# Performance work log

Measured on AMD Instinct MI355X. Metric: run time of the kernel, lower is better.

Reference implementation:

```python
import jax, jax.numpy as jnp
import numpy as np

SCALE = 1.0 / np.sqrt(3.0)  # head dim is input_dim = 3


def setup_inputs() -> dict:
    key = jax.random.key(0)
    ks = jax.random.split(key, 7)
    B, Nq, Nf, D, C = 4, 2048, 16384, 3, 768
    return {
        "q": jax.random.normal(ks[0], (B, Nq, D), dtype=jnp.float32),
        "k": jax.random.normal(ks[1], (B, Nf, D), dtype=jnp.float32),
        "v": jax.random.normal(ks[2], (B, Nf, C), dtype=jnp.float32),
        "W1": jax.random.normal(ks[3], (D, D), dtype=jnp.float32) * (1.0 / np.sqrt(D)),
        "b1": jax.random.normal(ks[4], (D,), dtype=jnp.float32) * 0.01,
        "W2": jax.random.normal(ks[5], (D, D), dtype=jnp.float32) * (1.0 / np.sqrt(D)),
        "b2": jax.random.normal(ks[6], (D,), dtype=jnp.float32) * 0.01,
    }


def reference(q, k, v, W1, b1, W2, b2):
    # tiny per-point projections + ReLU (nn.Linear stores W as [out,in] -> x @ W.T + b)
    qp = jax.nn.relu(jnp.einsum("bnd,ed->bne", q, W1) + b1)  # [B, Nq, 3]
    kp = jax.nn.relu(jnp.einsum("bmd,ed->bme", k, W2) + b2)  # [B, Nf, 3]
    scores = jnp.einsum("bne,bme->bnm", qp, kp) * SCALE       # [B, Nq, Nf]
    attn = jax.nn.softmax(scores, axis=-1)
    return jnp.einsum("bnm,bmc->bnc", attn, v)                # [B, Nq, C]
```

## Files before the change

### kernel.cpp

```cpp
#include <hip/hip_runtime.h>
#include <math.h>

#define Bt  4
#define NQ  2048
#define NF  16384
#define CC  768

#define QT  128
#define CT  96
#define BK  128
#define THR 512
#define NCH (NF / BK)

#define NFS   4
#define KC    (NF / NFS)
#define BK2   16
#define NCH2  (KC / BK2)
#define TILEB (CC * BK2 * 2)
#define NTILE (Bt * (NF / BK2))

#define SCALE_LOG2E 0.8329080161227079f

typedef __attribute__((ext_vector_type(8)))  short  short8;
typedef __attribute__((ext_vector_type(4)))  float  floatx4;
typedef __attribute__((ext_vector_type(16))) float  floatx16;

#if __has_builtin(__builtin_amdgcn_exp2f)
#define EXP2F(x) __builtin_amdgcn_exp2f(x)
#else
#define EXP2F(x) __expf((x) * 0.6931471805599453f)
#endif

static __device__ __forceinline__ float relu(float x) { return fmaxf(x, 0.0f); }

static __device__ __forceinline__ unsigned int f2bf(float f) {
    unsigned int u = __float_as_uint(f);
    u += 0x7fffu + ((u >> 16) & 1u);
    return u >> 16;
}

#define GLDS16(gsrc, ldst)                                                        \
    __builtin_amdgcn_global_load_lds(                                             \
        (const __attribute__((address_space(1))) unsigned int*)(gsrc),            \
        (__attribute__((address_space(3))) unsigned int*)(ldst), 16, 0, 0)

__global__ __launch_bounds__(256) void prep_kernel(
    const float* __restrict__ q, const float* __restrict__ k,
    const float* __restrict__ W1, const float* __restrict__ b1,
    const float* __restrict__ W2, const float* __restrict__ b2,
    float4* __restrict__ qp, float* __restrict__ kp3)
{
    int idx = blockIdx.x * 256 + threadIdx.x;
    if (idx < Bt * NQ) {
        const float* r = q + (size_t)idx * 3;
        float x0 = r[0], x1 = r[1], x2 = r[2];
        float4 o;
        o.x = relu(fmaf(W1[0], x0, fmaf(W1[1], x1, fmaf(W1[2], x2, b1[0])))) * SCALE_LOG2E;
        o.y = relu(fmaf(W1[3], x0, fmaf(W1[4], x1, fmaf(W1[5], x2, b1[1])))) * SCALE_LOG2E;
        o.z = relu(fmaf(W1[6], x0, fmaf(W1[7], x1, fmaf(W1[8], x2, b1[2])))) * SCALE_LOG2E;
        o.w = 0.0f;
        qp[idx] = o;
    } else {
        int kidx = idx - Bt * NQ;
        const float* r = k + (size_t)kidx * 3;
        float x0 = r[0], x1 = r[1], x2 = r[2];
        float* dst = kp3 + (size_t)kidx * 3;
        dst[0] = relu(fmaf(W2[0], x0, fmaf(W2[1], x1, fmaf(W2[2], x2, b2[0]))));
        dst[1] = relu(fmaf(W2[3], x0, fmaf(W2[4], x1, fmaf(W2[5], x2, b2[1]))));
        dst[2] = relu(fmaf(W2[6], x0, fmaf(W2[7], x1, fmaf(W2[8], x2, b2[2]))));
    }
}

__global__ __launch_bounds__(256) void stats_kernel(
    float4* __restrict__ qp, const float* __restrict__ kp3,
    float2* __restrict__ rstat)
{
    __shared__ float wredA[4][16];
    __shared__ float wredB[4][16];

    const int bid  = blockIdx.x;
    const int b    = bid >> 7;
    const int q0   = (bid & 127) * 16;
    const int t    = threadIdx.x;
    const int wv   = t >> 6;
    const int lane = t & 63;

    float qx[16], qy[16], qz[16];
#pragma unroll
    for (int i = 0; i < 16; ++i) {
        float4 qv = qp[b * NQ + q0 + i];
        qx[i] = qv.x; qy[i] = qv.y; qz[i] = qv.z;
    }
    const float* kpb = kp3 + (size_t)b * NF * 3;

    float pmax[16];
#pragma unroll
    for (int i = 0; i < 16; ++i) pmax[i] = -1e30f;
    for (int m = t; m < NF; m += 256) {
        float kx = kpb[3 * m], ky = kpb[3 * m + 1], kz = kpb[3 * m + 2];
#pragma unroll
        for (int i = 0; i < 16; ++i) {
            float s = fmaf(qx[i], kx, fmaf(qy[i], ky, qz[i] * kz));
            pmax[i] = fmaxf(pmax[i], s);
        }
    }
#pragma unroll
    for (int off = 32; off >= 1; off >>= 1)
#pragma unroll
        for (int i = 0; i < 16; ++i)
            pmax[i] = fmaxf(pmax[i], __shfl_xor(pmax[i], off, 64));
    if (lane == 0)
#pragma unroll
        for (int i = 0; i < 16; ++i) wredA[wv][i] = pmax[i];
    __syncthreads();

    float rowmax[16];
#pragma unroll
    for (int i = 0; i < 16; ++i)
        rowmax[i] = fmaxf(fmaxf(wredA[0][i], wredA[1][i]),
                          fmaxf(wredA[2][i], wredA[3][i]));

    float psum[16];
#pragma unroll
    for (int i = 0; i < 16; ++i) psum[i] = 0.0f;
    for (int m = t; m < NF; m += 256) {
        float kx = kpb[3 * m], ky = kpb[3 * m + 1], kz = kpb[3 * m + 2];
#pragma unroll
        for (int i = 0; i < 16; ++i) {
            float s = fmaf(qx[i], kx, fmaf(qy[i], ky, qz[i] * kz));
            psum[i] += EXP2F(s - rowmax[i]);
        }
    }
#pragma unroll
    for (int off = 32; off >= 1; off >>= 1)
#pragma unroll
        for (int i = 0; i < 16; ++i)
            psum[i] += __shfl_xor(psum[i], off, 64);
    if (lane == 0)
#pragma unroll
        for (int i = 0; i < 16; ++i) wredB[wv][i] = psum[i];
    __syncthreads();

    if (t < 16) {
        float m = fmaxf(fmaxf(wredA[0][t], wredA[1][t]),
                        fmaxf(wredA[2][t], wredA[3][t]));
        float l = wredB[0][t] + wredB[1][t] + wredB[2][t] + wredB[3][t];
        int row = b * NQ + q0 + t;
        rstat[row] = make_float2(m, 1.0f / l);
        qp[row].w = -m;
    }
}

__global__ __launch_bounds__(256) void prep_v_kernel(
    const float* __restrict__ v, char* __restrict__ vpk)
{
    __shared__ float lt[16][132];
    const int t   = threadIdx.x;
    const int bid = blockIdx.x;
    const int cb  = bid % 6;
    const int ch  = (bid / 6) & 1023;
    const int b   = bid / (6 * 1024);
    const int c0  = cb * 128;

    const float* vb = v + ((size_t)b * NF + (size_t)ch * BK2) * CC + c0;
    const int c4 = (t & 31) * 4;
#pragma unroll
    for (int r2 = 0; r2 < 2; ++r2) {
        const int row = (t >> 5) + 8 * r2;
        *(float4*)&lt[row][c4] = *(const float4*)(vb + (size_t)row * CC + c4);
    }
    __syncthreads();

    const int c  = t >> 1;
    const int sl = t & 1;
    unsigned int dw[4];
#pragma unroll
    for (int i = 0; i < 4; ++i) {
        float a  = lt[8 * sl + 2 * i][c];
        float b2 = lt[8 * sl + 2 * i + 1][c];
        asm("v_cvt_pk_bf16_f32 %0, %1, %2" : "=v"(dw[i]) : "v"(a), "v"(b2));
    }
    const int cgl = c0 + c;
    char* dst = vpk + (size_t)(b * (NF / BK2) + ch) * TILEB
              + ((size_t)cgl << 5)
              + ((sl ^ ((cgl >> 2) & 1)) << 4);
    uint4 u; u.x = dw[0]; u.y = dw[1]; u.z = dw[2]; u.w = dw[3];
    *(uint4*)dst = u;
}

static __device__ __forceinline__ void produceA(
    const float* __restrict__ kpq,
    float qx, float qy, float qz, float qw,
    int l, int cg, unsigned int (*ab)[64][2])
{
    float2 a0 = *(const float2*)(kpq);
    float2 a1 = *(const float2*)(kpq + 2);
    float2 a2 = *(const float2*)(kpq + 4);
    float2 b0 = *(const float2*)(kpq + 24);
    float2 b1 = *(const float2*)(kpq + 26);
    float2 b2 = *(const float2*)(kpq + 28);
    float e0 = EXP2F(fmaf(qx, a0.x, fmaf(qy, a0.y, fmaf(qz, a1.x, qw))));
    float e1 = EXP2F(fmaf(qx, a1.y, fmaf(qy, a2.x, fmaf(qz, a2.y, qw))));
    float e2 = EXP2F(fmaf(qx, b0.x, fmaf(qy, b0.y, fmaf(qz, b1.x, qw))));
    float e3 = EXP2F(fmaf(qx, b1.y, fmaf(qy, b2.x, fmaf(qz, b2.y, qw))));
    unsigned int d0, d1;
    asm("v_cvt_pk_bf16_f32 %0, %1, %2" : "=v"(d0) : "v"(e0), "v"(e1));
    asm("v_cvt_pk_bf16_f32 %0, %1, %2" : "=v"(d1) : "v"(e2), "v"(e3));
    asm("v_permlane32_swap_b32 %0, %1" : "+v"(d0), "+v"(d1));
    ab[cg >> 1][l][cg & 1]       = d0;
    ab[(cg >> 1) + 2][l][cg & 1] = d1;
}

__global__ __launch_bounds__(256, 2) void attn_main32_kernel(
    const char* __restrict__ vpk, const float4* __restrict__ qp,
    const float* __restrict__ kp3, float* __restrict__ out,
    float* __restrict__ partial)
{
    __shared__ __align__(16) char vbuf[2][TILEB];
    __shared__ __align__(16) unsigned int abuf[2][4][64][2];

    const int t   = threadIdx.x;
    const int l   = t & 63;
    const int cg  = t >> 6;

    const int bid = blockIdx.x;
    const int g   = ((bid & 7) << 1) | ((bid >> 3) & 1);
    const int qt  = bid >> 4;
    const int b   = g >> 2;
    const int nfs = g & 3;

    const char*  vtile = vpk + (size_t)(b * (NF / BK2) + nfs * NCH2) * TILEB;
    const float* kpb   = kp3 + (size_t)(b * NF + nfs * KC) * 3;

    const float4 qv = qp[b * NQ + qt * 64 + l];
    const float qx = qv.x, qy = qv.y, qz = qv.z, qw = qv.w;

    floatx16 acc0[6], acc1[6];
#pragma unroll
    for (int cs = 0; cs < 6; ++cs)
#pragma unroll
        for (int r = 0; r < 16; ++r) { acc0[cs][r] = 0.0f; acc1[cs][r] = 0.0f; }

    const int lhi  = l >> 5;
    const int bofs = (cg * 192 + (l & 31)) * 32 + ((lhi ^ ((l >> 2) & 1)) << 4);

#define STAGE(CH, PB)                                                         \
    do {                                                                      \
        const char* src = vtile + (size_t)(CH) * TILEB + cg * 6144 + l * 16;  \
        char* dst = &vbuf[PB][cg * 6144];                                     \
        _Pragma("unroll")                                                     \
        for (int i = 0; i < 6; ++i) GLDS16(src + i * 1024, dst + i * 1024);   \
    } while (0)

    STAGE(0, 0);
    produceA(kpb + 6 * cg, qx, qy, qz, qw, l, cg, abuf[0]);

#pragma unroll 1
    for (int ch = 0; ch < NCH2; ++ch) {
        asm volatile("s_waitcnt vmcnt(0) lgkmcnt(0)" ::: "memory");
        __builtin_amdgcn_sched_barrier(0);
        __builtin_amdgcn_s_barrier();
        __builtin_amdgcn_sched_barrier(0);

        const int cur = ch & 1, nxt = cur ^ 1;
        if (ch + 1 < NCH2) STAGE(ch + 1, nxt);

        union { unsigned int u[4]; short8 s; } a0, a1;
        {
            const unsigned int (*AB)[64][2] = abuf[cur];
            uint2 p0 = *(const uint2*)&AB[0][l][0];
            uint2 p1 = *(const uint2*)&AB[1][l][0];
            uint2 p2 = *(const uint2*)&AB[2][l][0];
            uint2 p3 = *(const uint2*)&AB[3][l][0];
            a0.u[0] = p0.x; a0.u[1] = p0.y; a0.u[2] = p1.x; a0.u[3] = p1.y;
            a1.u[0] = p2.x; a1.u[1] = p2.y; a1.u[2] = p3.x; a1.u[3] = p3.y;
        }

        const char* bp = &vbuf[cur][0] + bofs;
        __builtin_amdgcn_s_setprio(1);
#pragma unroll
        for (int cs = 0; cs < 6; ++cs) {
            union { uint4 u; short8 s; } bw;
            bw.u = *(const uint4*)(bp + cs * 1024);
            acc0[cs] = __builtin_amdgcn_mfma_f32_32x32x16_bf16(a0.s, bw.s, acc0[cs], 0, 0, 0);
            acc1[cs] = __builtin_amdgcn_mfma_f32_32x32x16_bf16(a1.s, bw.s, acc1[cs], 0, 0, 0);
        }
        __builtin_amdgcn_s_setprio(0);

        if (ch + 1 < NCH2)
            produceA(kpb + (size_t)(ch + 1) * (BK2 * 3) + 6 * cg,
                     qx, qy, qz, qw, l, cg, abuf[nxt]);
    }
#undef STAGE

    float* obase = (nfs == 0) ? out
                 : (partial + (size_t)(nfs - 1) * ((size_t)Bt * NQ * CC));
    const int row0 = b * NQ + qt * 64 + 4 * lhi;
    const int col0 = cg * 192 + (l & 31);
#pragma unroll
    for (int cs = 0; cs < 6; ++cs)
#pragma unroll
        for (int r = 0; r < 16; ++r) {
            const int row = row0 + (r & 3) + 8 * (r >> 2);
            obase[(size_t)row * CC + col0 + cs * 32]        = acc0[cs][r];
            obase[(size_t)(row + 32) * CC + col0 + cs * 32] = acc1[cs][r];
        }
}

__global__ __launch_bounds__(256) void reduce_kernel(
    float* __restrict__ out, const float* __restrict__ part,
    const float2* __restrict__ rstat)
{
    const int TOT4 = Bt * NQ * CC / 4;
    float4* o4 = (float4*)out;
    const float4* p4 = (const float4*)part;
    for (int i = blockIdx.x * 256 + threadIdx.x; i < TOT4; i += gridDim.x * 256) {
        float4 o = o4[i];
        float4 a = p4[i], b2 = p4[TOT4 + i], c2 = p4[2 * TOT4 + i];
        float lv = rstat[i / (CC / 4)].y;
        o.x = (o.x + a.x + b2.x + c2.x) * lv;
        o.y = (o.y + a.y + b2.y + c2.y) * lv;
        o.z = (o.z + a.z + b2.z + c2.z) * lv;
        o.w = (o.w + a.w + b2.w + c2.w) * lv;
        o4[i] = o;
    }
}

__global__ __launch_bounds__(THR, 4) void attn_mfma_kernel(
    const float* __restrict__ v, const float4* __restrict__ qp,
    const float* __restrict__ kp3, const float2* __restrict__ rstat,
    float* __restrict__ out)
{
    __shared__ unsigned int vTd[2][CT * 68];
    __shared__ float4 kplB[2][96];

    const int t    = threadIdx.x;
    const int bid  = blockIdx.x;
    const int g    = (bid & 7) + 8 * ((bid >> 3) & 3);
    const int qt   = bid >> 5;
    const int b    = g >> 3;
    const int ct   = g & 7;

    const int lane = t & 63;
    const int wv   = t >> 6;
    const int quad = lane >> 4;
    const int l15  = lane & 15;

    const int qrow0 = b * NQ + qt * QT;
    const int cbase = ct * CT;

    float4 qv = qp[qrow0 + wv * 16 + l15];
    const float qx = qv.x, qy = qv.y, qz = qv.z, qw = qv.w;

    const int rp  = (t & 7) + 8 * wv;
    const int c4l = (t >> 3) & 7;

    const float*  vb   = v + (size_t)b * NF * CC + cbase;
    const float4* kp4g = (const float4*)(kp3 + (size_t)b * NF * 3);

    floatx4 acc[6];
#pragma unroll
    for (int cs = 0; cs < 6; ++cs) acc[cs] = (floatx4){0.f, 0.f, 0.f, 0.f};

    float va0[3][4], va1[3][4];
    float4 kpld = make_float4(0.f, 0.f, 0.f, 0.f);

#pragma unroll
    for (int rep = 0; rep < 3; ++rep) {
        int col = 4 * (c4l + 8 * rep);
        const float4* p0 = (const float4*)(vb + (size_t)(2 * rp) * CC + col);
        float4 a = p0[0];
        float4 bq = p0[CC / 4];
        va0[rep][0] = a.x;  va0[rep][1] = a.y;  va0[rep][2] = a.z;  va0[rep][3] = a.w;
        va1[rep][0] = bq.x; va1[rep][1] = bq.y; va1[rep][2] = bq.z; va1[rep][3] = bq.w;
    }
    if (t < 96) kpld = kp4g[t];

    for (int ch = 0; ch < NCH; ++ch) {
        const int p = ch & 1;
#pragma unroll
        for (int rep = 0; rep < 3; ++rep) {
            int c0 = 4 * (c4l + 8 * rep);
#pragma unroll
            for (int w = 0; w < 4; ++w) {
                unsigned int pk = f2bf(va0[rep][w]) | (f2bf(va1[rep][w]) << 16);
                vTd[p][(c0 + w) * 68 + (rp ^ (4 * c4l))] = pk;
            }
        }
        if (t < 96) kplB[p][t] = kpld;
        __syncthreads();

        if (ch + 1 < NCH) {
            int m0 = (ch + 1) * BK;
#pragma unroll
            for (int rep = 0; rep < 3; ++rep) {
                int col = 4 * (c4l + 8 * rep);
                const float4* p0 = (const float4*)(vb + (size_t)(m0 + 2 * rp) * CC + col);
                float4 a = p0[0];
                float4 bq = p0[CC / 4];
                va0[rep][0] = a.x;  va0[rep][1] = a.y;  va0[rep][2] = a.z;  va0[rep][3] = a.w;
                va1[rep][0] = bq.x; va1[rep][1] = bq.y; va1[rep][2] = bq.z; va1[rep][3] = bq.w;
            }
            if (t < 96) kpld = kp4g[(ch + 1) * 96 + t];
        }

#pragma unroll
        for (int kk = 0; kk < BK; kk += 32) {
            union { float4 v4[6]; float f[24]; } kq;
            const int kb4 = (kk * 3) / 4 + 6 * quad;
#pragma unroll
            for (int i = 0; i < 6; ++i) kq.v4[i] = kplB[p][kb4 + i];

            union { short8 s; unsigned int d[4]; } af;
#pragma unroll
            for (int j = 0; j < 8; j += 2) {
                float s0 = fmaf(qx, kq.f[3 * j],
                           fmaf(qy, kq.f[3 * j + 1],
                           fmaf(qz, kq.f[3 * j + 2], qw)));
                float s1 = fmaf(qx, kq.f[3 * j + 3],
                           fmaf(qy, kq.f[3 * j + 4],
                           fmaf(qz, kq.f[3 * j + 5], qw)));
                af.d[j >> 1] = f2bf(EXP2F(s0)) | (f2bf(EXP2F(s1)) << 16);
            }

#pragma unroll
            for (int cs = 0; cs < 6; ++cs) {
                int c  = cs * 16 + l15;
                int d0 = ((kk >> 1) + 4 * quad) ^ (4 * ((c >> 2) & 7));
                union { uint4 u; short8 s; } bw;
                bw.u = *(const uint4*)&vTd[p][c * 68 + d0];
                acc[cs] = __builtin_amdgcn_mfma_f32_16x16x32_bf16(
                    af.s, bw.s, acc[cs], 0, 0, 0);
            }
        }
        __syncthreads();
    }

#pragma unroll
    for (int vv = 0; vv < 4; ++vv) {
        int row = qrow0 + wv * 16 + quad * 4 + vv;
        float lv = rstat[row].y;
        float* orow = out + (size_t)row * CC + cbase + l15;
#pragma unroll
        for (int cs = 0; cs < 6; ++cs)
            orow[cs * 16] = acc[cs][vv] * lv;
    }
}

extern "C" void kernel_launch(void* const* d_in, const int* in_sizes, int n_in,
                              void* d_out, int out_size, void* d_ws, size_t ws_size,
                              hipStream_t stream) {
    const float* q  = (const float*)d_in[0];
    const float* k  = (const float*)d_in[1];
    const float* v  = (const float*)d_in[2];
    const float* W1 = (const float*)d_in[3];
    const float* b1 = (const float*)d_in[4];
    const float* W2 = (const float*)d_in[5];
    const float* b2 = (const float*)d_in[6];
    float* out = (float*)d_out;

    float*  kp3   = (float*)d_ws;
    float4* qpW   = (float4*)((char*)d_ws + (size_t)Bt * NF * 3 * 4);
    float2* rstat = (float2*)((char*)d_ws + (size_t)Bt * NF * 3 * 4 + (size_t)Bt * NQ * 16);
    char*   vpk   = (char*)d_ws + 983040;
    float*  part  = (float*)((char*)d_ws + 983040 + (size_t)NTILE * TILEB);
    const size_t need = 983040 + (size_t)NTILE * TILEB
                      + (size_t)3 * Bt * NQ * CC * 4;

    hipLaunchKernelGGL(prep_kernel, dim3((Bt * NQ + Bt * NF) / 256), dim3(256), 0, stream,
                       q, k, W1, b1, W2, b2, qpW, kp3);
    hipLaunchKernelGGL(stats_kernel, dim3(Bt * (NQ / 16)), dim3(256), 0, stream,
                       qpW, kp3, rstat);

    if (ws_size >= need) {
        hipLaunchKernelGGL(prep_v_kernel, dim3(Bt * (NF / BK2) * 6), dim3(256), 0, stream,
                           v, vpk);
        hipLaunchKernelGGL(attn_main32_kernel, dim3(Bt * 32 * NFS), dim3(256), 0, stream,
                           vpk, qpW, kp3, out, part);
        hipLaunchKernelGGL(reduce_kernel, dim3(2048), dim3(256), 0, stream,
                           out, part, rstat);
    } else {
        hipLaunchKernelGGL(attn_mfma_kernel, dim3(Bt * (NQ / QT) * (CC / CT)), dim3(THR), 0, stream,
                           v, qpW, kp3, rstat, out);
    }
}
```

Baseline: 743.3 us.

## Fuse softmax row sums into main kernel, widen blocks and triple-buffer V

Removes the separate stats kernel pass by accumulating the exp row sums inside the main MFMA kernel. These are written per split and combined and inverted in the reduce kernel. Blocks grow to 512 threads covering 128 query rows, so each staged V tile feeds twice as many rows. V staging is triple-buffered two chunks ahead, and the K loads for the next chunk are issued early into registers with partial vmcnt waits. The costs are more LDS, lower occupancy and fragile hand-counted waitcnt sequencing.

```diff
diff --git a/kernel.cpp b/kernel.cpp
--- a/kernel.cpp
+++ b/kernel.cpp
@@ -188,40 +188,20 @@
     *(uint4*)dst = u;
 }
 
-static __device__ __forceinline__ void produceA(
-    const float* __restrict__ kpq,
-    float qx, float qy, float qz, float qw,
-    int l, int cg, unsigned int (*ab)[64][2])
-{
-    float2 a0 = *(const float2*)(kpq);
-    float2 a1 = *(const float2*)(kpq + 2);
-    float2 a2 = *(const float2*)(kpq + 4);
-    float2 b0 = *(const float2*)(kpq + 24);
-    float2 b1 = *(const float2*)(kpq + 26);
-    float2 b2 = *(const float2*)(kpq + 28);
-    float e0 = EXP2F(fmaf(qx, a0.x, fmaf(qy, a0.y, fmaf(qz, a1.x, qw))));
-    float e1 = EXP2F(fmaf(qx, a1.y, fmaf(qy, a2.x, fmaf(qz, a2.y, qw))));
-    float e2 = EXP2F(fmaf(qx, b0.x, fmaf(qy, b0.y, fmaf(qz, b1.x, qw))));
-    float e3 = EXP2F(fmaf(qx, b1.y, fmaf(qy, b2.x, fmaf(qz, b2.y, qw))));
-    unsigned int d0, d1;
-    asm("v_cvt_pk_bf16_f32 %0, %1, %2" : "=v"(d0) : "v"(e0), "v"(e1));
-    asm("v_cvt_pk_bf16_f32 %0, %1, %2" : "=v"(d1) : "v"(e2), "v"(e3));
-    asm("v_permlane32_swap_b32 %0, %1" : "+v"(d0), "+v"(d1));
-    ab[cg >> 1][l][cg & 1]       = d0;
-    ab[(cg >> 1) + 2][l][cg & 1] = d1;
-}
-
-__global__ __launch_bounds__(256, 2) void attn_main32_kernel(
+__global__ __launch_bounds__(512) void attn_main32_kernel(
     const char* __restrict__ vpk, const float4* __restrict__ qp,
     const float* __restrict__ kp3, float* __restrict__ out,
-    float* __restrict__ partial)
+    float* __restrict__ partial, float* __restrict__ lpart)
 {
-    __shared__ __align__(16) char vbuf[2][TILEB];
-    __shared__ __align__(16) unsigned int abuf[2][4][64][2];
-
-    const int t   = threadIdx.x;
-    const int l   = t & 63;
-    const int cg  = t >> 6;
+    __shared__ __align__(16) char vbuf[3][TILEB];
+    __shared__ __align__(16) unsigned int abuf[2][2][4][64][2];
+    __shared__ float lred[2][4][64];
+
+    const int t  = threadIdx.x;
+    const int l  = t & 63;
+    const int wv = t >> 6;
+    const int wg = wv >> 2;
+    const int cg = wv & 3;
 
     const int bid = blockIdx.x;
     const int g   = ((bid & 7) << 1) | ((bid >> 3) & 1);
@@ -232,7 +212,7 @@
     const char*  vtile = vpk + (size_t)(b * (NF / BK2) + nfs * NCH2) * TILEB;
     const float* kpb   = kp3 + (size_t)(b * NF + nfs * KC) * 3;
 
-    const float4 qv = qp[b * NQ + qt * 64 + l];
+    const float4 qv = qp[b * NQ + qt * QT + wg * 64 + l];
     const float qx = qv.x, qy = qv.y, qz = qv.z, qw = qv.w;
 
     floatx16 acc0[6], acc1[6];
@@ -240,43 +220,87 @@
     for (int cs = 0; cs < 6; ++cs)
 #pragma unroll
         for (int r = 0; r < 16; ++r) { acc0[cs][r] = 0.0f; acc1[cs][r] = 0.0f; }
+
+    float lsum = 0.0f;
 
     const int lhi  = l >> 5;
     const int bofs = (cg * 192 + (l & 31)) * 32 + ((lhi ^ ((l >> 2) & 1)) << 4);
 
 #define STAGE(CH, PB)                                                         \
     do {                                                                      \
-        const char* src = vtile + (size_t)(CH) * TILEB + cg * 6144 + l * 16;  \
-        char* dst = &vbuf[PB][cg * 6144];                                     \
+        const char* src_ = vtile + (size_t)(CH) * TILEB + wv * 3072 + l * 16; \
+        char* dst_ = &vbuf[PB][wv * 3072];                                    \
         _Pragma("unroll")                                                     \
-        for (int i = 0; i < 6; ++i) GLDS16(src + i * 1024, dst + i * 1024);   \
+        for (int i_ = 0; i_ < 3; ++i_) GLDS16(src_ + i_ * 1024, dst_ + i_ * 1024); \
     } while (0)
 
-    STAGE(0, 0);
-    produceA(kpb + 6 * cg, qx, qy, qz, qw, l, cg, abuf[0]);
-
+#define KPLOAD(CH, R)                                                         \
+    do {                                                                      \
+        const float* p_ = kpb + (size_t)(CH) * (BK2 * 3) + 6 * cg;            \
+        asm volatile("global_load_dwordx2 %0, %6, off\n\t"                    \
+                     "global_load_dwordx2 %1, %6, off offset:8\n\t"           \
+                     "global_load_dwordx2 %2, %6, off offset:16\n\t"          \
+                     "global_load_dwordx2 %3, %6, off offset:96\n\t"          \
+                     "global_load_dwordx2 %4, %6, off offset:104\n\t"         \
+                     "global_load_dwordx2 %5, %6, off offset:112"             \
+                     : "=&v"(R[0]), "=&v"(R[1]), "=&v"(R[2]),                 \
+                       "=&v"(R[3]), "=&v"(R[4]), "=&v"(R[5])                  \
+                     : "v"(p_));                                              \
+    } while (0)
+
+#define PRODA(R, BB)                                                          \
+    do {                                                                      \
+        float e0_ = EXP2F(fmaf(qx, R[0].x, fmaf(qy, R[0].y, fmaf(qz, R[1].x, qw)))); \
+        float e1_ = EXP2F(fmaf(qx, R[1].y, fmaf(qy, R[2].x, fmaf(qz, R[2].y, qw)))); \
+        float e2_ = EXP2F(fmaf(qx, R[3].x, fmaf(qy, R[3].y, fmaf(qz, R[4].x, qw)))); \
+        float e3_ = EXP2F(fmaf(qx, R[4].y, fmaf(qy, R[5].x, fmaf(qz, R[5].y, qw)))); \
+        lsum += (e0_ + e1_) + (e2_ + e3_);                                    \
+        unsigned int d0_, d1_;                                                \
+        asm("v_cvt_pk_bf16_f32 %0, %1, %2" : "=v"(d0_) : "v"(e0_), "v"(e1_)); \
+        asm("v_cvt_pk_bf16_f32 %0, %1, %2" : "=v"(d1_) : "v"(e2_), "v"(e3_)); \
+        asm("v_permlane32_swap_b32 %0, %1" : "+v"(d0_), "+v"(d1_));           \
+        abuf[BB][wg][cg >> 1][l][cg & 1]       = d0_;                         \
+        abuf[BB][wg][(cg >> 1) + 2][l][cg & 1] = d1_;                         \
+    } while (0)
+
+    {
+        float2 kpr[6];
+        STAGE(0, 0);
+        STAGE(1, 1);
+        KPLOAD(0, kpr);
+        asm volatile("s_waitcnt vmcnt(0)" ::: "memory");
+        __builtin_amdgcn_sched_barrier(0);
+        PRODA(kpr, 0);
+    }
+
+    int p = 0;
 #pragma unroll 1
     for (int ch = 0; ch < NCH2; ++ch) {
-        asm volatile("s_waitcnt vmcnt(0) lgkmcnt(0)" ::: "memory");
+        asm volatile("s_waitcnt lgkmcnt(0)" ::: "memory");
         __builtin_amdgcn_sched_barrier(0);
         __builtin_amdgcn_s_barrier();
         __builtin_amdgcn_sched_barrier(0);
 
         const int cur = ch & 1, nxt = cur ^ 1;
-        if (ch + 1 < NCH2) STAGE(ch + 1, nxt);
+        float2 kpn[6];
+        if (ch + 1 < NCH2) KPLOAD(ch + 1, kpn);
+        if (ch + 2 < NCH2) {
+            const int p2 = (p + 2 >= 3) ? p + 2 - 3 : p + 2;
+            STAGE(ch + 2, p2);
+        }
+        __builtin_amdgcn_sched_barrier(0);
 
         union { unsigned int u[4]; short8 s; } a0, a1;
         {
-            const unsigned int (*AB)[64][2] = abuf[cur];
-            uint2 p0 = *(const uint2*)&AB[0][l][0];
-            uint2 p1 = *(const uint2*)&AB[1][l][0];
-            uint2 p2 = *(const uint2*)&AB[2][l][0];
-            uint2 p3 = *(const uint2*)&AB[3][l][0];
+            uint2 p0 = *(const uint2*)&abuf[cur][wg][0][l][0];
+            uint2 p1 = *(const uint2*)&abuf[cur][wg][1][l][0];
+            uint2 p2v = *(const uint2*)&abuf[cur][wg][2][l][0];
+            uint2 p3 = *(const uint2*)&abuf[cur][wg][3][l][0];
             a0.u[0] = p0.x; a0.u[1] = p0.y; a0.u[2] = p1.x; a0.u[3] = p1.y;
-            a1.u[0] = p2.x; a1.u[1] = p2.y; a1.u[2] = p3.x; a1.u[3] = p3.y;
-        }
-
-        const char* bp = &vbuf[cur][0] + bofs;
+            a1.u[0] = p2v.x; a1.u[1] = p2v.y; a1.u[2] = p3.x; a1.u[3] = p3.y;
+        }
+        const char* bp = &vbuf[p][0] + bofs;
+
         __builtin_amdgcn_s_setprio(1);
 #pragma unroll
         for (int cs = 0; cs < 6; ++cs) {
@@ -286,16 +310,30 @@
             acc1[cs] = __builtin_amdgcn_mfma_f32_32x32x16_bf16(a1.s, bw.s, acc1[cs], 0, 0, 0);
         }
         __builtin_amdgcn_s_setprio(0);
-
-        if (ch + 1 < NCH2)
-            produceA(kpb + (size_t)(ch + 1) * (BK2 * 3) + 6 * cg,
-                     qx, qy, qz, qw, l, cg, abuf[nxt]);
+        __builtin_amdgcn_sched_barrier(0);
+
+        if (ch + 1 < NCH2) {
+            if (ch + 2 < NCH2) asm volatile("s_waitcnt vmcnt(3)" ::: "memory");
+            else               asm volatile("s_waitcnt vmcnt(0)" ::: "memory");
+            __builtin_amdgcn_sched_barrier(0);
+            PRODA(kpn, nxt);
+        }
+        p = (p + 1 == 3) ? 0 : p + 1;
     }
 #undef STAGE
+#undef KPLOAD
+#undef PRODA
+
+    lred[wg][cg][l] = lsum;
+    __syncthreads();
+    if (cg == 0) {
+        float tot = lred[wg][0][l] + lred[wg][1][l] + lred[wg][2][l] + lred[wg][3][l];
+        lpart[(size_t)nfs * (Bt * NQ) + b * NQ + qt * QT + wg * 64 + l] = tot;
+    }
 
     float* obase = (nfs == 0) ? out
                  : (partial + (size_t)(nfs - 1) * ((size_t)Bt * NQ * CC));
-    const int row0 = b * NQ + qt * 64 + 4 * lhi;
+    const int row0 = b * NQ + qt * QT + wg * 64 + 4 * lhi;
     const int col0 = cg * 192 + (l & 31);
 #pragma unroll
     for (int cs = 0; cs < 6; ++cs)
@@ -309,15 +347,18 @@
 
 __global__ __launch_bounds__(256) void reduce_kernel(
     float* __restrict__ out, const float* __restrict__ part,
-    const float2* __restrict__ rstat)
+    const float* __restrict__ lpart)
 {
     const int TOT4 = Bt * NQ * CC / 4;
+    const int NROW = Bt * NQ;
     float4* o4 = (float4*)out;
     const float4* p4 = (const float4*)part;
     for (int i = blockIdx.x * 256 + threadIdx.x; i < TOT4; i += gridDim.x * 256) {
         float4 o = o4[i];
         float4 a = p4[i], b2 = p4[TOT4 + i], c2 = p4[2 * TOT4 + i];
-        float lv = rstat[i / (CC / 4)].y;
+        int row = i / (CC / 4);
+        float lv = 1.0f / (lpart[row] + lpart[NROW + row]
+                         + lpart[2 * NROW + row] + lpart[3 * NROW + row]);
         o.x = (o.x + a.x + b2.x + c2.x) * lv;
         o.y = (o.y + a.y + b2.y + c2.y) * lv;
         o.z = (o.z + a.z + b2.z + c2.z) * lv;
@@ -461,25 +502,26 @@
 
     float*  kp3   = (float*)d_ws;
     float4* qpW   = (float4*)((char*)d_ws + (size_t)Bt * NF * 3 * 4);
-    float2* rstat = (float2*)((char*)d_ws + (size_t)Bt * NF * 3 * 4 + (size_t)Bt * NQ * 16);
-    char*   vpk   = (char*)d_ws + 983040;
-    float*  part  = (float*)((char*)d_ws + 983040 + (size_t)NTILE * TILEB);
-    const size_t need = 983040 + (size_t)NTILE * TILEB
+    float*  lpart = (float*)((char*)d_ws + 917504);
+    float2* rstat = (float2*)((char*)d_ws + 917504);
+    char*   vpk   = (char*)d_ws + 1048576;
+    float*  part  = (float*)((char*)d_ws + 1048576 + (size_t)NTILE * TILEB);
+    const size_t need = 1048576 + (size_t)NTILE * TILEB
                       + (size_t)3 * Bt * NQ * CC * 4;
 
     hipLaunchKernelGGL(prep_kernel, dim3((Bt * NQ + Bt * NF) / 256), dim3(256), 0, stream,
                        q, k, W1, b1, W2, b2, qpW, kp3);
-    hipLaunchKernelGGL(stats_kernel, dim3(Bt * (NQ / 16)), dim3(256), 0, stream,
-                       qpW, kp3, rstat);
 
     if (ws_size >= need) {
         hipLaunchKernelGGL(prep_v_kernel, dim3(Bt * (NF / BK2) * 6), dim3(256), 0, stream,
                            v, vpk);
-        hipLaunchKernelGGL(attn_main32_kernel, dim3(Bt * 32 * NFS), dim3(256), 0, stream,
-                           vpk, qpW, kp3, out, part);
+        hipLaunchKernelGGL(attn_main32_kernel, dim3(Bt * 16 * NFS), dim3(512), 0, stream,
+                           vpk, qpW, kp3, out, part, lpart);
         hipLaunchKernelGGL(reduce_kernel, dim3(2048), dim3(256), 0, stream,
-                           out, part, rstat);
+                           out, part, lpart);
     } else {
+        hipLaunchKernelGGL(stats_kernel, dim3(Bt * (NQ / 16)), dim3(256), 0, stream,
+                           qpW, kp3, rstat);
         hipLaunchKernelGGL(attn_mfma_kernel, dim3(Bt * (NQ / QT) * (CC / CT)), dim3(THR), 0, stream,
                            v, qpW, kp3, rstat, out);
     }
```

Result: faster. 667.8 us (-10.2%).
